# Optimization experiments

Hardware: AMD Instinct MI355X
Metric: run time of the kernel (lower is better)

## Reference

```python
import jax, jax.numpy as jnp
import numpy as np

B, D, H, E, K = 8192, 1024, 256, 16, 4


def setup_inputs() -> dict:
    key = jax.random.key(0)
    ks = jax.random.split(key, 6)
    s_d = D ** -0.5
    s_h = H ** -0.5
    return {
        "x": jax.random.normal(ks[0], (B, D), dtype=jnp.float32),
        "route_w": jax.random.normal(ks[1], (E, D), dtype=jnp.float32) * s_d,
        "w1": jax.random.normal(ks[2], (E, H, D), dtype=jnp.float32) * s_d,
        "b1": jax.random.normal(ks[3], (E, H), dtype=jnp.float32) * s_d,
        "w2": jax.random.normal(ks[4], (E, D, H), dtype=jnp.float32) * s_h,
        "b2": jax.random.normal(ks[5], (E, D), dtype=jnp.float32) * s_h,
    }


def _moe_forward(x, route_w, w1, b1, w2, b2):
    # Router: logits (B, E) -> top-k softmax weights scattered back to (B, E).
    logits = x @ route_w.T
    top_vals, top_idx = jax.lax.top_k(logits, K)
    top_w = jax.nn.softmax(top_vals, axis=-1)
    rows = jnp.arange(x.shape[0])[:, None]
    weights = jnp.zeros_like(logits).at[rows, top_idx].set(top_w)  # (B, E)

    # Experts: out = sum_e w[:, e] * relu(relu(x W1e^T + b1e) W2e^T + b2e)
    # Non-selected experts have weight 0, so dense-then-weight matches the
    # original masked gather/scatter math exactly (dropout = 0).
    def step(out, params_e):
        W1, bb1, W2, bb2, we = params_e
        h = jax.nn.relu(x @ W1.T + bb1)       # (B, H)
        y = jax.nn.relu(h @ W2.T + bb2)       # (B, D)
        return out + y * we[:, None], None

    out0 = jnp.zeros_like(x)
    out, _ = jax.lax.scan(step, out0, (w1, b1, w2, b2, weights.T))
    return out


def reference(x, route_w, w1, b1, w2, b2):
    return _moe_forward(x, route_w, w1, b1, w2, b2)
```

## Files before the change

kernel.cpp:

```cpp
#include <hip/hip_runtime.h>
#include <stdint.h>

typedef unsigned short u16;
typedef __attribute__((ext_vector_type(8))) short bf16x8;
typedef __attribute__((ext_vector_type(4))) float f32x4;
typedef __attribute__((ext_vector_type(8))) u16 u16x8;
typedef __attribute__((ext_vector_type(4))) u16 u16x4;
typedef __attribute__((ext_vector_type(2))) double f64x2;

#define NTOK 8192
#define DDIM 1024
#define HDIM 256
#define NEXP 16
#define MAXT 272
#define MAXSLOT (MAXT * 128)

__device__ __forceinline__ u16 f2bf(float f) {
  uint32_t u = __builtin_bit_cast(uint32_t, f);
  u += 0x7FFFu + ((u >> 16) & 1u);
  return (u16)(u >> 16);
}
__device__ __forceinline__ float bf2f(u16 h) {
  return __builtin_bit_cast(float, (uint32_t)h << 16);
}

__device__ __forceinline__ void gll16(const void* g, void* l) {
  __builtin_amdgcn_global_load_lds((const __attribute__((address_space(1))) void*)g,
                                   (__attribute__((address_space(3))) void*)l,
                                   16, 0, 0);
}

__global__ __launch_bounds__(256) void cvt_kernel(const float* __restrict__ in,
                                                  u16* __restrict__ out) {
  size_t i = ((size_t)blockIdx.x * 256 + threadIdx.x) * 8;
  const float4 a = *(const float4*)(in + i);
  const float4 b = *(const float4*)(in + i + 4);
  u16x8 o;
  o[0] = f2bf(a.x); o[1] = f2bf(a.y); o[2] = f2bf(a.z); o[3] = f2bf(a.w);
  o[4] = f2bf(b.x); o[5] = f2bf(b.y); o[6] = f2bf(b.z); o[7] = f2bf(b.w);
  *(u16x8*)(out + i) = o;
}

__global__ __launch_bounds__(256) void zero_out_kernel(float* __restrict__ p) {
  size_t i = ((size_t)blockIdx.x * 256 + threadIdx.x) * 4;
  *(float4*)(p + i) = (float4){0.f, 0.f, 0.f, 0.f};
}

__global__ __launch_bounds__(256) void rwd_kernel(const float* __restrict__ rw,
                                                  double* __restrict__ rwd) {
  int i = blockIdx.x * 256 + threadIdx.x;
  rwd[i] = (double)rw[i];
}

__global__ __launch_bounds__(256) void router_kernel(const float* __restrict__ x,
                                                     const double* __restrict__ rwd,
                                                     int* __restrict__ epack,
                                                     float* __restrict__ ew,
                                                     u16* __restrict__ xbf) {
  const int wid = threadIdx.x >> 6, lane = threadIdx.x & 63;
  const int b = blockIdx.x * 4 + wid;
  const float* xrow = x + (size_t)b * DDIM;

  double acc[NEXP];
#pragma unroll
  for (int e = 0; e < NEXP; ++e) acc[e] = 0.0;

#pragma unroll
  for (int i = 0; i < 4; ++i) {
    const int d = lane * 4 + i * 256;
    float4 xv = *(const float4*)(xrow + d);
    u16x4 o;
    o[0] = f2bf(xv.x); o[1] = f2bf(xv.y); o[2] = f2bf(xv.z); o[3] = f2bf(xv.w);
    *(u16x4*)(xbf + (size_t)b * DDIM + d) = o;
    const double x0 = xv.x, x1 = xv.y, x2 = xv.z, x3 = xv.w;
#pragma unroll
    for (int e = 0; e < NEXP; ++e) {
      const double* rp = rwd + e * DDIM + d;
      f64x2 r0 = *(const f64x2*)rp;
      f64x2 r1 = *(const f64x2*)(rp + 2);
      acc[e] = fma(x0, r0[0], acc[e]);
      acc[e] = fma(x1, r0[1], acc[e]);
      acc[e] = fma(x2, r1[0], acc[e]);
      acc[e] = fma(x3, r1[1], acc[e]);
    }
  }

#define FOLD(H, M)                                                   \
  _Pragma("unroll") for (int i = 0; i < H; ++i) {                    \
    double send = (lane & M) ? acc[i] : acc[i + H];                  \
    double recv = __shfl_xor(send, M);                               \
    acc[i] = ((lane & M) ? acc[i + H] : acc[i]) + recv;              \
  }
  FOLD(8, 1)
  FOLD(4, 2)
  FOLD(2, 4)
  FOLD(1, 8)
#undef FOLD
  acc[0] += __shfl_xor(acc[0], 16);
  acc[0] += __shfl_xor(acc[0], 32);
  const int e_mine = ((lane & 1) << 3) | ((lane & 2) << 1) |
                     ((lane & 4) >> 1) | ((lane & 8) >> 3);

  double val = acc[0];
  double tv[4]; int tidx[4];
#pragma unroll
  for (int k = 0; k < 4; ++k) {
    double bv = val; int be = e_mine;
#pragma unroll
    for (int m = 1; m < 16; m <<= 1) {
      double ov = __shfl_xor(bv, m);
      int oe = __shfl_xor(be, m);
      if (ov > bv || (ov == bv && oe < be)) { bv = ov; be = oe; }
    }
    tv[k] = bv; tidx[k] = be;
    if (e_mine == be) val = -1.0e300;
  }

  if (lane == 0) {
    float m0 = (float)tv[0];
    float w[4]; float s = 0.f;
#pragma unroll
    for (int k = 0; k < 4; ++k) { w[k] = expf((float)tv[k] - m0); s += w[k]; }
    epack[b] = tidx[0] | (tidx[1] << 8) | (tidx[2] << 16) | (tidx[3] << 24);
#pragma unroll
    for (int k = 0; k < 4; ++k) ew[b * 4 + k] = w[k] / s;
  }
}

__global__ __launch_bounds__(1024) void compact_kernel(const int* __restrict__ epack,
                                                       const float* __restrict__ ew,
                                                       int* __restrict__ texp,
                                                       int* __restrict__ perm,
                                                       float* __restrict__ wsl,
                                                       int* __restrict__ islot) {
  __shared__ int wave_cnt[16][NEXP];
  __shared__ int counts_sm[NEXP];
  __shared__ int wtot[16], wave_off[16];
  const int e = blockIdx.x;
  const int tid = threadIdx.x, lane = tid & 63, w = tid >> 6;

  int ep[8]; unsigned m[8];
#pragma unroll
  for (int j = 0; j < 8; ++j) {
    ep[j] = epack[tid * 8 + j];
    m[j] = (1u << (ep[j] & 255)) | (1u << ((ep[j] >> 8) & 255)) |
           (1u << ((ep[j] >> 16) & 255)) | (1u << ((ep[j] >> 24) & 255));
  }
#pragma unroll
  for (int ee = 0; ee < NEXP; ++ee) {
    int c = 0;
#pragma unroll
    for (int j = 0; j < 8; ++j) c += (m[j] >> ee) & 1u;
#pragma unroll
    for (int off = 32; off > 0; off >>= 1) c += __shfl_xor(c, off);
    if (lane == 0) wave_cnt[w][ee] = c;
  }
  unsigned fm = 0;
#pragma unroll
  for (int j = 0; j < 8; ++j) fm |= ((m[j] >> e) & 1u) << j;
  int s = __popc(fm);
  int incl = s;
#pragma unroll
  for (int d = 1; d < 64; d <<= 1) {
    int t2 = __shfl_up(incl, d);
    if (lane >= d) incl += t2;
  }
  if (lane == 63) wtot[w] = incl;
  __syncthreads();
  if (tid < NEXP) {
    int c = 0;
    for (int w2 = 0; w2 < 16; ++w2) c += wave_cnt[w2][tid];
    counts_sm[tid] = c;
  }
  if (tid == 0) {
    int run = 0;
    for (int w2 = 0; w2 < 16; ++w2) { wave_off[w2] = run; run += wtot[w2]; }
  }
  __syncthreads();
  int base = 0;
  for (int ee = 0; ee < NEXP; ++ee)
    if (ee < e) base += ((counts_sm[ee] + 127) >> 7) << 7;
  int pos = base + wave_off[w] + (incl - s);
#pragma unroll
  for (int j = 0; j < 8; ++j) {
    if ((fm >> j) & 1u) {
      int tok = tid * 8 + j;
      int b0 = ep[j] & 255, b1 = (ep[j] >> 8) & 255, b2_ = (ep[j] >> 16) & 255;
      int k = (b0 == e) ? 0 : ((b1 == e) ? 1 : ((b2_ == e) ? 2 : 3));
      perm[pos] = tok;
      wsl[pos] = ew[tok * 4 + k];
      islot[tok * 4 + k] = pos;
      ++pos;
    }
  }
  int cnt = counts_sm[e];
  int pad = (((cnt + 127) >> 7) << 7) - cnt;
  if (tid < pad) { perm[base + cnt + tid] = 0; wsl[base + cnt + tid] = 0.f; }
  if (e == 0 && tid == 0) {
    int tc = 0;
    for (int ee = 0; ee < NEXP; ++ee) {
      int nt = (counts_sm[ee] + 127) >> 7;
      for (int i = 0; i < nt; ++i) texp[tc++] = ee;
    }
    for (; tc < MAXT; ++tc) texp[tc] = -1;
  }
}

__device__ __forceinline__ void stage_rows(const u16* __restrict__ base, int ld,
                                           int kbase, uint8_t* dst, int tid) {
#pragma unroll
  for (int i = 0; i < 4; ++i) {
    int u = i * 256 + tid;
    int row = u >> 3, g = u & 7;
    gll16(base + (size_t)row * ld + kbase + ((g ^ (row & 7)) << 3), dst + u * 16);
  }
}
__device__ __forceinline__ void stage_gather(const u16* __restrict__ xbf,
                                             const int tok[4], int kbase,
                                             uint8_t* dst, int tid) {
#pragma unroll
  for (int i = 0; i < 4; ++i) {
    int u = i * 256 + tid;
    int row = u >> 3, g = u & 7;
    gll16(xbf + (size_t)tok[i] * DDIM + kbase + ((g ^ (row & 7)) << 3), dst + u * 16);
  }
}

__device__ __forceinline__ void mma_tile(const uint8_t* Ab, const uint8_t* Bb,
                                         f32x4 acc[4][4], int wm, int wn,
                                         int lrow, int lk) {
#pragma unroll
  for (int s = 0; s < 2; ++s) {
    bf16x8 af[4], bfr[4];
#pragma unroll
    for (int f = 0; f < 4; ++f) {
      int ar = wm * 64 + f * 16 + lrow;
      af[f] = *(const bf16x8*)(Ab + ar * 128 + ((((s << 2) | lk) ^ (ar & 7)) << 4));
      int br = wn * 64 + f * 16 + lrow;
      bfr[f] = *(const bf16x8*)(Bb + br * 128 + ((((s << 2) | lk) ^ (br & 7)) << 4));
    }
#pragma unroll
    for (int i = 0; i < 4; ++i)
#pragma unroll
      for (int j = 0; j < 4; ++j)
        acc[i][j] = __builtin_amdgcn_mfma_f32_16x16x32_bf16(af[i], bfr[j], acc[i][j], 0, 0, 0);
  }
}

__global__ __launch_bounds__(256) void gemm1_kernel(const u16* __restrict__ xbf,
                                                    const u16* __restrict__ w1bf,
                                                    const float* __restrict__ b1,
                                                    const int* __restrict__ texp,
                                                    const int* __restrict__ perm,
                                                    u16* __restrict__ Hc, int t0) {
  __shared__ __align__(16) uint8_t smem[2][32768];
  const int t = t0 + blockIdx.x;
  const int e = (t < MAXT) ? texp[t] : -1;
  if (e < 0) return;
  const int n0 = blockIdx.y * 128;
  const int tid = threadIdx.x;
  const int lane = tid & 63, wid = tid >> 6;
  const int wm = wid >> 1, wn = wid & 1;
  const int lrow = lane & 15, lk = lane >> 4;

  int tok[4];
#pragma unroll
  for (int i = 0; i < 4; ++i) tok[i] = perm[t * 128 + ((i * 256 + tid) >> 3)];
  const u16* Bsrc = w1bf + ((size_t)e * HDIM + n0) * DDIM;

  f32x4 acc[4][4];
#pragma unroll
  for (int i = 0; i < 4; ++i)
#pragma unroll
    for (int j = 0; j < 4; ++j) acc[i][j] = (f32x4){0.f, 0.f, 0.f, 0.f};

  stage_gather(xbf, tok, 0, smem[0], tid);
  stage_rows(Bsrc, DDIM, 0, smem[0] + 16384, tid);
  __syncthreads();
  int cur = 0;
  for (int kt = 0; kt < 16; ++kt) {
    if (kt < 15) {
      stage_gather(xbf, tok, (kt + 1) * 64, smem[cur ^ 1], tid);
      stage_rows(Bsrc, DDIM, (kt + 1) * 64, smem[cur ^ 1] + 16384, tid);
    }
    mma_tile(smem[cur], smem[cur] + 16384, acc, wm, wn, lrow, lk);
    __syncthreads();
    cur ^= 1;
  }
#pragma unroll
  for (int j = 0; j < 4; ++j) {
    int n = n0 + wn * 64 + j * 16 + lrow;
    float bias = b1[e * HDIM + n];
#pragma unroll
    for (int i = 0; i < 4; ++i) {
      int rloc = blockIdx.x * 128 + wm * 64 + i * 16 + lk * 4;
#pragma unroll
      for (int r = 0; r < 4; ++r) {
        float h = fmaxf(acc[i][j][r] + bias, 0.f);
        Hc[((size_t)rloc + r) * HDIM + n] = f2bf(h);
      }
    }
  }
}

template <int MODE>
__global__ __launch_bounds__(256) void gemm2_kernel(const u16* __restrict__ Hc,
                                                    const u16* __restrict__ w2bf,
                                                    const float* __restrict__ b2,
                                                    const int* __restrict__ texp,
                                                    const int* __restrict__ perm,
                                                    const float* __restrict__ wsl,
                                                    float* __restrict__ out,
                                                    u16* __restrict__ ybuf,
                                                    int t0, int n0, int NC) {
  __shared__ __align__(16) uint8_t smem[2][32768];
  const int t = t0 + blockIdx.x;
  const int e = (t < MAXT) ? texp[t] : -1;
  if (e < 0) return;
  const int tid = threadIdx.x;
  const int lane = tid & 63, wid = tid >> 6;
  const int wm = wid >> 1, wn = wid & 1;
  const int lrow = lane & 15, lk = lane >> 4;

  const u16* Asrc = Hc + (size_t)blockIdx.x * 128 * HDIM;
  const u16* Bsrc = w2bf + ((size_t)e * DDIM + n0 + blockIdx.y * 128) * HDIM;

  f32x4 acc[4][4];
#pragma unroll
  for (int i = 0; i < 4; ++i)
#pragma unroll
    for (int j = 0; j < 4; ++j) acc[i][j] = (f32x4){0.f, 0.f, 0.f, 0.f};

  stage_rows(Asrc, HDIM, 0, smem[0], tid);
  stage_rows(Bsrc, HDIM, 0, smem[0] + 16384, tid);
  __syncthreads();
  int cur = 0;
  for (int kt = 0; kt < 4; ++kt) {
    if (kt < 3) {
      stage_rows(Asrc, HDIM, (kt + 1) * 64, smem[cur ^ 1], tid);
      stage_rows(Bsrc, HDIM, (kt + 1) * 64, smem[cur ^ 1] + 16384, tid);
    }
    mma_tile(smem[cur], smem[cur] + 16384, acc, wm, wn, lrow, lk);
    __syncthreads();
    cur ^= 1;
  }
  float bias[4];
#pragma unroll
  for (int j = 0; j < 4; ++j)
    bias[j] = b2[e * DDIM + n0 + blockIdx.y * 128 + wn * 64 + j * 16 + lrow];
#pragma unroll
  for (int i = 0; i < 4; ++i) {
#pragma unroll
    for (int r = 0; r < 4; ++r) {
      int slot = t * 128 + wm * 64 + i * 16 + lk * 4 + r;
      if (MODE == 0) {
        int tokn = perm[slot];
        float w = wsl[slot];
#pragma unroll
        for (int j = 0; j < 4; ++j) {
          int n = n0 + blockIdx.y * 128 + wn * 64 + j * 16 + lrow;
          float h = fmaxf(acc[i][j][r] + bias[j], 0.f);
          atomicAdd(&out[(size_t)tokn * DDIM + n], w * h);
        }
      } else {
#pragma unroll
        for (int j = 0; j < 4; ++j) {
          int nloc = blockIdx.y * 128 + wn * 64 + j * 16 + lrow;
          float h = fmaxf(acc[i][j][r] + bias[j], 0.f);
          ybuf[(size_t)slot * NC + nloc] = f2bf(h);
        }
      }
    }
  }
}

__global__ __launch_bounds__(256) void combine_kernel(const u16* __restrict__ ybuf,
                                                      const float* __restrict__ ew,
                                                      const int* __restrict__ islot,
                                                      float* __restrict__ out,
                                                      int n0, int NC, int cshift) {
  int gid = blockIdx.x * 256 + threadIdx.x;
  int t = gid >> cshift;
  int c = (gid & ((1 << cshift) - 1)) << 2;
  const int4 sl = *(const int4*)(islot + t * 4);
  const float4 w = *(const float4*)(ew + t * 4);
  float4 a = {0.f, 0.f, 0.f, 0.f};
#define ACC(SL, W)                                             \
  {                                                            \
    u16x4 y = *(const u16x4*)(ybuf + (size_t)(SL)*NC + c);     \
    a.x += (W)*bf2f(y[0]); a.y += (W)*bf2f(y[1]);              \
    a.z += (W)*bf2f(y[2]); a.w += (W)*bf2f(y[3]);              \
  }
  ACC(sl.x, w.x); ACC(sl.y, w.y); ACC(sl.z, w.z); ACC(sl.w, w.w);
#undef ACC
  *(float4*)(out + (size_t)t * DDIM + n0 + c) = a;
}

extern "C" void kernel_launch(void* const* d_in, const int* in_sizes, int n_in,
                              void* d_out, int out_size, void* d_ws, size_t ws_size,
                              hipStream_t stream) {
  const float* x = (const float*)d_in[0];
  const float* route_w = (const float*)d_in[1];
  const float* w1 = (const float*)d_in[2];
  const float* b1 = (const float*)d_in[3];
  const float* w2 = (const float*)d_in[4];
  const float* b2 = (const float*)d_in[5];
  float* out = (float*)d_out;

  uint8_t* ws = (uint8_t*)d_ws;
  const size_t OFF_EPACK = 0;
  const size_t OFF_EW    = 32768;
  const size_t OFF_ISLOT = 163840;
  const size_t OFF_TEXP  = 294912;
  const size_t OFF_PERM  = 296960;
  const size_t OFF_WSL   = 436224;
  const size_t OFF_RWD   = 786432;
  const size_t OFF_X     = 1048576;
  const size_t OFF_W1    = OFF_X + (size_t)NTOK * DDIM * 2;
  const size_t OFF_W2    = OFF_W1 + (size_t)NEXP * HDIM * DDIM * 2;
  const size_t OFF_HC    = OFF_W2 + (size_t)NEXP * DDIM * HDIM * 2;
  const size_t OFF_Y     = OFF_HC + (size_t)MAXSLOT * HDIM * 2;

  int* epack  = (int*)(ws + OFF_EPACK);
  float* ew   = (float*)(ws + OFF_EW);
  int* islot  = (int*)(ws + OFF_ISLOT);
  int* texp   = (int*)(ws + OFF_TEXP);
  int* perm   = (int*)(ws + OFF_PERM);
  float* wsl  = (float*)(ws + OFF_WSL);
  double* rwd = (double*)(ws + OFF_RWD);
  u16* xbf    = (u16*)(ws + OFF_X);
  u16* w1bf   = (u16*)(ws + OFF_W1);
  u16* w2bf   = (u16*)(ws + OFF_W2);
  u16* Hc     = (u16*)(ws + OFF_HC);
  u16* ybuf   = (u16*)(ws + OFF_Y);

  rwd_kernel<<<dim3((NEXP * DDIM) / 256), 256, 0, stream>>>(route_w, rwd);
  cvt_kernel<<<dim3((NEXP * HDIM * DDIM) / 2048), 256, 0, stream>>>(w1, w1bf);
  cvt_kernel<<<dim3((NEXP * DDIM * HDIM) / 2048), 256, 0, stream>>>(w2, w2bf);
  router_kernel<<<dim3(NTOK / 4), 256, 0, stream>>>(x, rwd, epack, ew, xbf);
  compact_kernel<<<dim3(NEXP), 1024, 0, stream>>>(epack, ew, texp, perm, wsl, islot);

  int NC = 0;
  for (int cand = 1024; cand >= 128; cand >>= 1) {
    if (ws_size >= OFF_Y + (size_t)MAXSLOT * cand * 2) { NC = cand; break; }
  }

  if (NC > 0) {
    gemm1_kernel<<<dim3(MAXT, HDIM / 128), 256, 0, stream>>>(xbf, w1bf, b1, texp, perm, Hc, 0);
    int cshift = __builtin_ctz(NC >> 2);
    for (int n0 = 0; n0 < DDIM; n0 += NC) {
      gemm2_kernel<1><<<dim3(MAXT, NC / 128), 256, 0, stream>>>(
          Hc, w2bf, b2, texp, perm, wsl, out, ybuf, 0, n0, NC);
      combine_kernel<<<dim3((NTOK << cshift) / 256), 256, 0, stream>>>(
          ybuf, ew, islot, out, n0, NC, cshift);
    }
  } else {
    long room = (long)ws_size - (long)OFF_HC;
    int CT = (int)(room / 65536);
    if (CT > MAXT) CT = MAXT;
    if (CT < 16) CT = 16;
    zero_out_kernel<<<dim3((NTOK * DDIM) / 1024), 256, 0, stream>>>(out);
    for (int t0 = 0; t0 < MAXT; t0 += CT) {
      int ct = (MAXT - t0 < CT) ? (MAXT - t0) : CT;
      gemm1_kernel<<<dim3(ct, HDIM / 128), 256, 0, stream>>>(xbf, w1bf, b1, texp, perm, Hc, t0);
      gemm2_kernel<0><<<dim3(ct, DDIM / 128), 256, 0, stream>>>(
          Hc, w2bf, b2, texp, perm, wsl, out, ybuf, t0, 0, DDIM);
    }
  }
}
```

Measured before the change: 169.1 us.

## Stage router weights in LDS and process four tokens per wave

Removes the separate fp64 conversion kernel for the router weights. The router now stages the fp32 router weights in shared memory once per block and has each wave handle four tokens, so every weight load is reused across four tokens' double-precision FMAs. This cuts global weight traffic and one kernel launch. In exchange it uses 64KB of LDS per block, quadruples the accumulator registers, and launches fewer blocks, which may lower occupancy.

```diff
diff --git a/kernel.cpp b/kernel.cpp
--- a/kernel.cpp
+++ b/kernel.cpp
@@ -6,7 +6,6 @@
 typedef __attribute__((ext_vector_type(4))) float f32x4;
 typedef __attribute__((ext_vector_type(8))) u16 u16x8;
 typedef __attribute__((ext_vector_type(4))) u16 u16x4;
-typedef __attribute__((ext_vector_type(2))) double f64x2;
 
 #define NTOK 8192
 #define DDIM 1024
@@ -46,84 +45,99 @@
   *(float4*)(p + i) = (float4){0.f, 0.f, 0.f, 0.f};
 }
 
-__global__ __launch_bounds__(256) void rwd_kernel(const float* __restrict__ rw,
-                                                  double* __restrict__ rwd) {
-  int i = blockIdx.x * 256 + threadIdx.x;
-  rwd[i] = (double)rw[i];
-}
-
 __global__ __launch_bounds__(256) void router_kernel(const float* __restrict__ x,
-                                                     const double* __restrict__ rwd,
+                                                     const float* __restrict__ rw,
                                                      int* __restrict__ epack,
                                                      float* __restrict__ ew,
                                                      u16* __restrict__ xbf) {
-  const int wid = threadIdx.x >> 6, lane = threadIdx.x & 63;
-  const int b = blockIdx.x * 4 + wid;
-  const float* xrow = x + (size_t)b * DDIM;
-
-  double acc[NEXP];
-#pragma unroll
-  for (int e = 0; e < NEXP; ++e) acc[e] = 0.0;
+  __shared__ __align__(16) float rwlds[NEXP * DDIM];
+  const int tid = threadIdx.x;
+  const int wid = tid >> 6, lane = tid & 63;
+
+#pragma unroll
+  for (int i = 0; i < 16; ++i) {
+    int idx = (i * 256 + tid) * 4;
+    *(float4*)(rwlds + idx) = *(const float4*)(rw + idx);
+  }
+  __syncthreads();
+
+  const int tb = blockIdx.x * 16 + wid * 4;
+
+  double acc[4][NEXP];
+#pragma unroll
+  for (int t = 0; t < 4; ++t)
+#pragma unroll
+    for (int e = 0; e < NEXP; ++e) acc[t][e] = 0.0;
 
 #pragma unroll
   for (int i = 0; i < 4; ++i) {
     const int d = lane * 4 + i * 256;
-    float4 xv = *(const float4*)(xrow + d);
-    u16x4 o;
-    o[0] = f2bf(xv.x); o[1] = f2bf(xv.y); o[2] = f2bf(xv.z); o[3] = f2bf(xv.w);
-    *(u16x4*)(xbf + (size_t)b * DDIM + d) = o;
-    const double x0 = xv.x, x1 = xv.y, x2 = xv.z, x3 = xv.w;
+    double xd[4][4];
+#pragma unroll
+    for (int t = 0; t < 4; ++t) {
+      float4 xv = *(const float4*)(x + (size_t)(tb + t) * DDIM + d);
+      u16x4 o;
+      o[0] = f2bf(xv.x); o[1] = f2bf(xv.y); o[2] = f2bf(xv.z); o[3] = f2bf(xv.w);
+      *(u16x4*)(xbf + (size_t)(tb + t) * DDIM + d) = o;
+      xd[t][0] = xv.x; xd[t][1] = xv.y; xd[t][2] = xv.z; xd[t][3] = xv.w;
+    }
 #pragma unroll
     for (int e = 0; e < NEXP; ++e) {
-      const double* rp = rwd + e * DDIM + d;
-      f64x2 r0 = *(const f64x2*)rp;
-      f64x2 r1 = *(const f64x2*)(rp + 2);
-      acc[e] = fma(x0, r0[0], acc[e]);
-      acc[e] = fma(x1, r0[1], acc[e]);
-      acc[e] = fma(x2, r1[0], acc[e]);
-      acc[e] = fma(x3, r1[1], acc[e]);
-    }
-  }
-
-#define FOLD(H, M)                                                   \
-  _Pragma("unroll") for (int i = 0; i < H; ++i) {                    \
-    double send = (lane & M) ? acc[i] : acc[i + H];                  \
-    double recv = __shfl_xor(send, M);                               \
-    acc[i] = ((lane & M) ? acc[i + H] : acc[i]) + recv;              \
-  }
-  FOLD(8, 1)
-  FOLD(4, 2)
-  FOLD(2, 4)
-  FOLD(1, 8)
-#undef FOLD
-  acc[0] += __shfl_xor(acc[0], 16);
-  acc[0] += __shfl_xor(acc[0], 32);
+      float4 rv = *(const float4*)(rwlds + e * DDIM + d);
+      const double r0 = rv.x, r1 = rv.y, r2 = rv.z, r3 = rv.w;
+#pragma unroll
+      for (int t = 0; t < 4; ++t) {
+        acc[t][e] = fma(xd[t][0], r0, acc[t][e]);
+        acc[t][e] = fma(xd[t][1], r1, acc[t][e]);
+        acc[t][e] = fma(xd[t][2], r2, acc[t][e]);
+        acc[t][e] = fma(xd[t][3], r3, acc[t][e]);
+      }
+    }
+  }
+
   const int e_mine = ((lane & 1) << 3) | ((lane & 2) << 1) |
                      ((lane & 4) >> 1) | ((lane & 8) >> 3);
 
-  double val = acc[0];
-  double tv[4]; int tidx[4];
-#pragma unroll
-  for (int k = 0; k < 4; ++k) {
-    double bv = val; int be = e_mine;
-#pragma unroll
-    for (int m = 1; m < 16; m <<= 1) {
-      double ov = __shfl_xor(bv, m);
-      int oe = __shfl_xor(be, m);
-      if (ov > bv || (ov == bv && oe < be)) { bv = ov; be = oe; }
-    }
-    tv[k] = bv; tidx[k] = be;
-    if (e_mine == be) val = -1.0e300;
-  }
-
-  if (lane == 0) {
-    float m0 = (float)tv[0];
-    float w[4]; float s = 0.f;
-#pragma unroll
-    for (int k = 0; k < 4; ++k) { w[k] = expf((float)tv[k] - m0); s += w[k]; }
-    epack[b] = tidx[0] | (tidx[1] << 8) | (tidx[2] << 16) | (tidx[3] << 24);
-#pragma unroll
-    for (int k = 0; k < 4; ++k) ew[b * 4 + k] = w[k] / s;
+#pragma unroll
+  for (int t = 0; t < 4; ++t) {
+#define FOLD(H, M)                                                     \
+  _Pragma("unroll") for (int i = 0; i < H; ++i) {                      \
+    double send = (lane & M) ? acc[t][i] : acc[t][i + H];              \
+    double recv = __shfl_xor(send, M);                                 \
+    acc[t][i] = ((lane & M) ? acc[t][i + H] : acc[t][i]) + recv;       \
+  }
+    FOLD(8, 1)
+    FOLD(4, 2)
+    FOLD(2, 4)
+    FOLD(1, 8)
+#undef FOLD
+    acc[t][0] += __shfl_xor(acc[t][0], 16);
+    acc[t][0] += __shfl_xor(acc[t][0], 32);
+
+    double val = acc[t][0];
+    double tv[4]; int tidx[4];
+#pragma unroll
+    for (int k = 0; k < 4; ++k) {
+      double bv = val; int be = e_mine;
+#pragma unroll
+      for (int m = 1; m < 16; m <<= 1) {
+        double ov = __shfl_xor(bv, m);
+        int oe = __shfl_xor(be, m);
+        if (ov > bv || (ov == bv && oe < be)) { bv = ov; be = oe; }
+      }
+      tv[k] = bv; tidx[k] = be;
+      if (e_mine == be) val = -1.0e300;
+    }
+
+    if (lane == 0) {
+      float m0 = (float)tv[0];
+      float w[4]; float s = 0.f;
+#pragma unroll
+      for (int k = 0; k < 4; ++k) { w[k] = expf((float)tv[k] - m0); s += w[k]; }
+      epack[tb + t] = tidx[0] | (tidx[1] << 8) | (tidx[2] << 16) | (tidx[3] << 24);
+#pragma unroll
+      for (int k = 0; k < 4; ++k) ew[(tb + t) * 4 + k] = w[k] / s;
+    }
   }
 }
 
@@ -414,7 +428,6 @@
   const size_t OFF_TEXP  = 294912;
   const size_t OFF_PERM  = 296960;
   const size_t OFF_WSL   = 436224;
-  const size_t OFF_RWD   = 786432;
   const size_t OFF_X     = 1048576;
   const size_t OFF_W1    = OFF_X + (size_t)NTOK * DDIM * 2;
   const size_t OFF_W2    = OFF_W1 + (size_t)NEXP * HDIM * DDIM * 2;
@@ -427,17 +440,15 @@
   int* texp   = (int*)(ws + OFF_TEXP);
   int* perm   = (int*)(ws + OFF_PERM);
   float* wsl  = (float*)(ws + OFF_WSL);
-  double* rwd = (double*)(ws + OFF_RWD);
   u16* xbf    = (u16*)(ws + OFF_X);
   u16* w1bf   = (u16*)(ws + OFF_W1);
   u16* w2bf   = (u16*)(ws + OFF_W2);
   u16* Hc     = (u16*)(ws + OFF_HC);
   u16* ybuf   = (u16*)(ws + OFF_Y);
 
-  rwd_kernel<<<dim3((NEXP * DDIM) / 256), 256, 0, stream>>>(route_w, rwd);
   cvt_kernel<<<dim3((NEXP * HDIM * DDIM) / 2048), 256, 0, stream>>>(w1, w1bf);
   cvt_kernel<<<dim3((NEXP * DDIM * HDIM) / 2048), 256, 0, stream>>>(w2, w2bf);
-  router_kernel<<<dim3(NTOK / 4), 256, 0, stream>>>(x, rwd, epack, ew, xbf);
+  router_kernel<<<dim3(NTOK / 16), 256, 0, stream>>>(x, route_w, epack, ew, xbf);
   compact_kernel<<<dim3(NEXP), 1024, 0, stream>>>(epack, ew, texp, perm, wsl, islot);
 
   int NC = 0;
```

Result: slower. 226.6 us (+34.0%).

## Stage router weights in swizzled LDS and process 16 tokens per block

Applied to the files above, without the earlier changes.

Removes the separate kernel that widened router weights to double. The router now stages the fp32 router weights (64 KB) into swizzled shared memory once per block and converts them to double in registers. Each wave now handles four tokens, 16 lanes per token, which drops two cross-lane reduction steps. The cost is a 64 KB LDS allocation per block, which limits occupancy, plus a per-block weight load that is repeated across 512 blocks.

```diff
diff --git a/kernel.cpp b/kernel.cpp
--- a/kernel.cpp
+++ b/kernel.cpp
@@ -6,7 +6,6 @@
 typedef __attribute__((ext_vector_type(4))) float f32x4;
 typedef __attribute__((ext_vector_type(8))) u16 u16x8;
 typedef __attribute__((ext_vector_type(4))) u16 u16x4;
-typedef __attribute__((ext_vector_type(2))) double f64x2;
 
 #define NTOK 8192
 #define DDIM 1024
@@ -46,42 +45,48 @@
   *(float4*)(p + i) = (float4){0.f, 0.f, 0.f, 0.f};
 }
 
-__global__ __launch_bounds__(256) void rwd_kernel(const float* __restrict__ rw,
-                                                  double* __restrict__ rwd) {
-  int i = blockIdx.x * 256 + threadIdx.x;
-  rwd[i] = (double)rw[i];
-}
-
 __global__ __launch_bounds__(256) void router_kernel(const float* __restrict__ x,
-                                                     const double* __restrict__ rwd,
+                                                     const float* __restrict__ rw,
                                                      int* __restrict__ epack,
                                                      float* __restrict__ ew,
                                                      u16* __restrict__ xbf) {
-  const int wid = threadIdx.x >> 6, lane = threadIdx.x & 63;
-  const int b = blockIdx.x * 4 + wid;
-  const float* xrow = x + (size_t)b * DDIM;
+  __shared__ __align__(16) uint8_t rwlds[65536];
+  const int tid = threadIdx.x;
+
+#pragma unroll
+  for (int i = 0; i < 16; ++i) {
+    int byte = (i * 256 + tid) * 16;
+    int sw = byte ^ (((byte >> 8) & 7) << 4);
+    *(float4*)(rwlds + sw) = *(const float4*)((const uint8_t*)rw + byte);
+  }
+  __syncthreads();
+
+  const int lane = tid & 63, wid = tid >> 6;
+  const int s = lane & 15;
+  const int tok = blockIdx.x * 16 + wid * 4 + (lane >> 4);
+  const float* xrow = x + (size_t)tok * DDIM;
+  u16* xbrow = xbf + (size_t)tok * DDIM;
 
   double acc[NEXP];
 #pragma unroll
   for (int e = 0; e < NEXP; ++e) acc[e] = 0.0;
 
-#pragma unroll
-  for (int i = 0; i < 4; ++i) {
-    const int d = lane * 4 + i * 256;
+#pragma unroll 4
+  for (int g = 0; g < 16; ++g) {
+    const int d = s * 64 + g * 4;
     float4 xv = *(const float4*)(xrow + d);
     u16x4 o;
     o[0] = f2bf(xv.x); o[1] = f2bf(xv.y); o[2] = f2bf(xv.z); o[3] = f2bf(xv.w);
-    *(u16x4*)(xbf + (size_t)b * DDIM + d) = o;
+    *(u16x4*)(xbrow + d) = o;
     const double x0 = xv.x, x1 = xv.y, x2 = xv.z, x3 = xv.w;
+    const int roff = (s * 256 + g * 16) ^ ((s & 7) << 4);
 #pragma unroll
     for (int e = 0; e < NEXP; ++e) {
-      const double* rp = rwd + e * DDIM + d;
-      f64x2 r0 = *(const f64x2*)rp;
-      f64x2 r1 = *(const f64x2*)(rp + 2);
-      acc[e] = fma(x0, r0[0], acc[e]);
-      acc[e] = fma(x1, r0[1], acc[e]);
-      acc[e] = fma(x2, r1[0], acc[e]);
-      acc[e] = fma(x3, r1[1], acc[e]);
+      float4 rv = *(const float4*)(rwlds + e * 4096 + roff);
+      acc[e] = fma(x0, (double)rv.x, acc[e]);
+      acc[e] = fma(x1, (double)rv.y, acc[e]);
+      acc[e] = fma(x2, (double)rv.z, acc[e]);
+      acc[e] = fma(x3, (double)rv.w, acc[e]);
     }
   }
 
@@ -96,8 +101,6 @@
   FOLD(2, 4)
   FOLD(1, 8)
 #undef FOLD
-  acc[0] += __shfl_xor(acc[0], 16);
-  acc[0] += __shfl_xor(acc[0], 32);
   const int e_mine = ((lane & 1) << 3) | ((lane & 2) << 1) |
                      ((lane & 4) >> 1) | ((lane & 8) >> 3);
 
@@ -116,14 +119,14 @@
     if (e_mine == be) val = -1.0e300;
   }
 
-  if (lane == 0) {
+  if ((lane & 15) == 0) {
     float m0 = (float)tv[0];
-    float w[4]; float s = 0.f;
-#pragma unroll
-    for (int k = 0; k < 4; ++k) { w[k] = expf((float)tv[k] - m0); s += w[k]; }
-    epack[b] = tidx[0] | (tidx[1] << 8) | (tidx[2] << 16) | (tidx[3] << 24);
-#pragma unroll
-    for (int k = 0; k < 4; ++k) ew[b * 4 + k] = w[k] / s;
+    float w[4]; float sum = 0.f;
+#pragma unroll
+    for (int k = 0; k < 4; ++k) { w[k] = expf((float)tv[k] - m0); sum += w[k]; }
+    epack[tok] = tidx[0] | (tidx[1] << 8) | (tidx[2] << 16) | (tidx[3] << 24);
+#pragma unroll
+    for (int k = 0; k < 4; ++k) ew[tok * 4 + k] = w[k] / sum;
   }
 }
 
@@ -414,7 +417,6 @@
   const size_t OFF_TEXP  = 294912;
   const size_t OFF_PERM  = 296960;
   const size_t OFF_WSL   = 436224;
-  const size_t OFF_RWD   = 786432;
   const size_t OFF_X     = 1048576;
   const size_t OFF_W1    = OFF_X + (size_t)NTOK * DDIM * 2;
   const size_t OFF_W2    = OFF_W1 + (size_t)NEXP * HDIM * DDIM * 2;
@@ -427,17 +429,15 @@
   int* texp   = (int*)(ws + OFF_TEXP);
   int* perm   = (int*)(ws + OFF_PERM);
   float* wsl  = (float*)(ws + OFF_WSL);
-  double* rwd = (double*)(ws + OFF_RWD);
   u16* xbf    = (u16*)(ws + OFF_X);
   u16* w1bf   = (u16*)(ws + OFF_W1);
   u16* w2bf   = (u16*)(ws + OFF_W2);
   u16* Hc     = (u16*)(ws + OFF_HC);
   u16* ybuf   = (u16*)(ws + OFF_Y);
 
-  rwd_kernel<<<dim3((NEXP * DDIM) / 256), 256, 0, stream>>>(route_w, rwd);
   cvt_kernel<<<dim3((NEXP * HDIM * DDIM) / 2048), 256, 0, stream>>>(w1, w1bf);
   cvt_kernel<<<dim3((NEXP * DDIM * HDIM) / 2048), 256, 0, stream>>>(w2, w2bf);
-  router_kernel<<<dim3(NTOK / 4), 256, 0, stream>>>(x, rwd, epack, ew, xbf);
+  router_kernel<<<dim3(NTOK / 16), 256, 0, stream>>>(x, route_w, epack, ew, xbf);
   compact_kernel<<<dim3(NEXP), 1024, 0, stream>>>(epack, ew, texp, perm, wsl, islot);
 
   int NC = 0;
```

After: 145.3 us. 14.1% less time.
